# Kernel tuning notes

Measured on AMD Instinct MI355X. Metric: run time of the kernel, lower is better.

The kernel has to match this reference:

```python
import jax, jax.numpy as jnp
import numpy as np

EMBED_DIM = 1024
NUM_HEADS = 16


def setup_inputs() -> dict:
    key = jax.random.key(0)
    k_x, k_qw, k_qb, k_pw, k_bias, k_mask = jax.random.split(key, 6)
    B, N, C = 2, 2048, EMBED_DIM
    x = jax.random.normal(k_x, (B, N, C), dtype=jnp.float32)
    # torch Linear params: weight (out,in), bias (out,)
    qkv_w = jax.random.normal(k_qw, (3 * C, C), dtype=jnp.float32) * (C ** -0.5)
    qkv_b = jax.random.normal(k_qb, (3 * C,), dtype=jnp.float32) * 0.02
    proj_w = jax.random.normal(k_pw, (C, C), dtype=jnp.float32) * (C ** -0.5)
    proj_b = jnp.zeros((C,), dtype=jnp.float32)
    # nn.Parameter(torch.zeros(H,1,1)); small noise so the bias is non-trivial
    physics_bias = jax.random.normal(k_bias, (NUM_HEADS, 1, 1), dtype=jnp.float32) * 0.01
    physics_mask = jax.random.randint(k_mask, (B, 1, N, N), 0, 2).astype(jnp.int32)
    return {"x": x, "qkv_w": qkv_w, "qkv_b": qkv_b, "proj_w": proj_w,
            "proj_b": proj_b, "physics_bias": physics_bias,
            "physics_mask": physics_mask}


def reference(x, qkv_w, qkv_b, proj_w, proj_b, physics_bias, physics_mask):
    B, N, C = x.shape
    H = NUM_HEADS
    Dh = C // H
    # fused QKV projection: (B,N,3C) -> (B,N,3,H,Dh)
    qkv = (x @ qkv_w.T + qkv_b).reshape(B, N, 3, H, Dh)
    q = jnp.transpose(qkv[:, :, 0], (0, 2, 1, 3))  # (B,H,N,Dh)
    k = jnp.transpose(qkv[:, :, 1], (0, 2, 1, 3))
    v = jnp.transpose(qkv[:, :, 2], (0, 2, 1, 3))
    scale = Dh ** -0.5
    attn = jnp.einsum('bhnd,bhmd->bhnm', q, k) * scale  # (B,H,N,N)
    attn = attn + physics_bias  # (H,1,1) broadcasts per head
    attn = jnp.where(physics_mask == 0, -jnp.inf, attn)
    attn = jax.nn.softmax(attn, axis=-1)
    out = jnp.einsum('bhnm,bhmd->bhnd', attn, v)  # (B,H,N,Dh)
    out = jnp.transpose(out, (0, 2, 1, 3)).reshape(B, N, C)
    return out @ proj_w.T + proj_b
```

## Files before the change

### kernel.cpp

```cpp
#include <hip/hip_runtime.h>
#include <hip/hip_bf16.h>
#include <stdint.h>
#include <math.h>


typedef __bf16 bf16;
typedef __bf16 bf16x8 __attribute__((ext_vector_type(8)));
typedef __bf16 bf16x4 __attribute__((ext_vector_type(4)));
typedef float f32x4 __attribute__((ext_vector_type(4)));
typedef float f32x16 __attribute__((ext_vector_type(16)));

#define MFMA(a,b,c) __builtin_amdgcn_mfma_f32_16x16x32_bf16((a),(b),(c),0,0,0)
#define MFMA32(a,b,c) __builtin_amdgcn_mfma_f32_32x32x16_bf16((a),(b),(c),0,0,0)
#define L2E 1.44269504f

#if __has_builtin(__builtin_amdgcn_exp2f)
#define EXP2(x) __builtin_amdgcn_exp2f(x)
#else
#define EXP2(x) exp2f(x)
#endif

__device__ __forceinline__ void async16(const void* g, void* l) {
  __builtin_amdgcn_global_load_lds(
      (const __attribute__((address_space(1))) void*)g,
      (__attribute__((address_space(3))) void*)l, 16, 0, 0);
}

template <bool F32>
__device__ __forceinline__ bf16x8 ld8(const void* base, size_t off) {
  if constexpr (F32) {
    const float* p = (const float*)base + off;
    float4 u = *(const float4*)p;
    float4 v = *(const float4*)(p + 4);
    bf16x8 r;
    r[0] = (bf16)u.x; r[1] = (bf16)u.y; r[2] = (bf16)u.z; r[3] = (bf16)u.w;
    r[4] = (bf16)v.x; r[5] = (bf16)v.y; r[6] = (bf16)v.z; r[7] = (bf16)v.w;
    return r;
  } else {
    return *(const bf16x8*)((const bf16*)base + off);
  }
}

__global__ __launch_bounds__(256) void prep(const int* __restrict__ mask,
                                            unsigned long long* __restrict__ mbg,
                                            const float* __restrict__ x, bf16* __restrict__ xb,
                                            const float* __restrict__ qw, bf16* __restrict__ qwb,
                                            const float* __restrict__ pw, bf16* __restrict__ pwb) {
  int bid = blockIdx.x, tid = threadIdx.x;
  if (bid < 4096) {
    int lane = tid & 63, wv = tid >> 6;
    const int* mrow = mask + (size_t)bid * 2048;
#pragma unroll
    for (int i = 0; i < 8; ++i) {
      int w = wv * 8 + i;
      unsigned long long bal = __ballot(mrow[w * 64 + lane] != 0);
      if (lane == 0) mbg[(size_t)bid * 32 + w] = bal;
    }
  } else if (bid < 6144) {
    size_t i = ((size_t)(bid - 4096) * 256 + tid) * 8;
    *(bf16x8*)&xb[i] = ld8<true>(x, i);
  } else if (bid < 7680) {
    size_t i = ((size_t)(bid - 6144) * 256 + tid) * 8;
    *(bf16x8*)&qwb[i] = ld8<true>(qw, i);
  } else {
    size_t i = ((size_t)(bid - 7680) * 256 + tid) * 8;
    *(bf16x8*)&pwb[i] = ld8<true>(pw, i);
  }
}

template <bool AF32, bool BF32>
__device__ __forceinline__ void gemm_core(const void* __restrict__ A,
                                          const void* __restrict__ B,
                                          int m0, int n0,
                                          f32x4 acc[4][4],
                                          bf16* Al, bf16* Bl) {
  const int K = 1024;
  int tid = threadIdx.x, lane = tid & 63, wv = tid >> 6;
  int wm = wv & 1, wn = wv >> 1, g = lane >> 4, li = lane & 15;
  int r8 = lane >> 3, c8 = lane & 7;

  for (int kt = 0; kt < K; kt += 64) {
    if constexpr (!AF32 && !BF32) {
      const bf16* Ab = (const bf16*)A;
      const bf16* Bb = (const bf16*)B;
      __syncthreads();
#pragma unroll
      for (int i2 = 0; i2 < 4; ++i2) {
        int rb = wv * 32 + i2 * 8;
        async16(&Ab[(size_t)(m0 + rb + r8) * K + kt + c8 * 8], &Al[rb * 64]);
        async16(&Bb[(size_t)(n0 + rb + r8) * K + kt + c8 * 8], &Bl[rb * 64]);
      }
      __syncthreads();
    } else {
      bf16x8 ta[4], tb[4];
#pragma unroll
      for (int i2 = 0; i2 < 4; ++i2) {
        int row = wv * 32 + i2 * 8 + r8;
        ta[i2] = ld8<AF32>(A, (size_t)(m0 + row) * K + kt + c8 * 8);
        tb[i2] = ld8<BF32>(B, (size_t)(n0 + row) * K + kt + c8 * 8);
      }
      __syncthreads();
#pragma unroll
      for (int i2 = 0; i2 < 4; ++i2) {
        int row = wv * 32 + i2 * 8 + r8;
        *(bf16x8*)&Al[row * 64 + c8 * 8] = ta[i2];
        *(bf16x8*)&Bl[row * 64 + c8 * 8] = tb[i2];
      }
      __syncthreads();
    }
#pragma unroll
    for (int ks = 0; ks < 64; ks += 32) {
      bf16x8 af[4], bg[4];
#pragma unroll
      for (int i = 0; i < 4; ++i)
        af[i] = *(const bf16x8*)&Al[(wm * 64 + i * 16 + li) * 64 + ks + g * 8];
#pragma unroll
      for (int j = 0; j < 4; ++j)
        bg[j] = *(const bf16x8*)&Bl[(wn * 64 + j * 16 + li) * 64 + ks + g * 8];
#pragma unroll
      for (int i = 0; i < 4; ++i)
#pragma unroll
        for (int j = 0; j < 4; ++j)
          acc[i][j] = MFMA(af[i], bg[j], acc[i][j]);
    }
  }
}

__device__ __forceinline__ void epi_qk(f32x4 acc[4][4], int m0, int n0,
                                       const float* __restrict__ bias,
                                       bf16* __restrict__ qg, bf16* __restrict__ kg) {
  int lane = threadIdx.x & 63, wv = threadIdx.x >> 6;
  int wm = wv & 1, wn = wv >> 1, g = lane >> 4, li = lane & 15;
#pragma unroll
  for (int i = 0; i < 4; ++i) {
    int o = m0 + wm * 64 + i * 16 + g * 4;
    int s = o >> 10, h = (o >> 6) & 15, d = o & 63;
    float sc = s ? 1.0f : 0.125f * L2E;
    float b0 = bias[o], b1 = bias[o + 1], b2 = bias[o + 2], b3 = bias[o + 3];
    bf16* dstb = s ? kg : qg;
#pragma unroll
    for (int j = 0; j < 4; ++j) {
      int t = n0 + wn * 64 + j * 16 + li;
      int b = t >> 11, n = t & 2047;
      ushort4 pk;
      ((bf16*)&pk)[0] = (bf16)((acc[i][j][0] + b0) * sc);
      ((bf16*)&pk)[1] = (bf16)((acc[i][j][1] + b1) * sc);
      ((bf16*)&pk)[2] = (bf16)((acc[i][j][2] + b2) * sc);
      ((bf16*)&pk)[3] = (bf16)((acc[i][j][3] + b3) * sc);
      *(ushort4*)&dstb[(((size_t)b * 16 + h) * 2048 + n) * 64 + d] = pk;
    }
  }
}

__device__ __forceinline__ void epi_v(f32x4 acc[4][4], int m0, int n0,
                                      const float* __restrict__ bias,
                                      bf16* __restrict__ vtg) {
  int lane = threadIdx.x & 63, wvv = threadIdx.x >> 6;
  int wm = wvv & 1, wn = wvv >> 1, g = lane >> 4, li = lane & 15;
#pragma unroll
  for (int i = 0; i < 4; ++i) {
    int t = m0 + wm * 64 + i * 16 + g * 4;
    int b = t >> 11, n = t & 2047;
#pragma unroll
    for (int j = 0; j < 4; ++j) {
      int ov = n0 + wn * 64 + j * 16 + li;
      int h = ov >> 6, d = ov & 63;
      float bv = bias[ov];
      ushort4 pk;
      ((bf16*)&pk)[0] = (bf16)(acc[i][j][0] + bv);
      ((bf16*)&pk)[1] = (bf16)(acc[i][j][1] + bv);
      ((bf16*)&pk)[2] = (bf16)(acc[i][j][2] + bv);
      ((bf16*)&pk)[3] = (bf16)(acc[i][j][3] + bv);
      *(ushort4*)&vtg[(((size_t)b * 16 + h) * 64 + d) * 2048 + n] = pk;
    }
  }
}

__global__ __launch_bounds__(256) void gemm_qkv(const bf16* __restrict__ xb,
                                                const bf16* __restrict__ qwb,
                                                const float* __restrict__ bias,
                                                bf16* __restrict__ qg,
                                                bf16* __restrict__ kg,
                                                bf16* __restrict__ vtg) {
  __shared__ bf16 Al[128 * 64], Bl[128 * 64];
  f32x4 acc[4][4];
#pragma unroll
  for (int i = 0; i < 4; ++i)
#pragma unroll
    for (int j = 0; j < 4; ++j) acc[i][j] = (f32x4){0.f, 0.f, 0.f, 0.f};
  int bid = blockIdx.x;
  if (bid < 512) {
    int m0 = (bid >> 5) * 128, n0 = (bid & 31) * 128;
    gemm_core<false, false>(qwb, xb, m0, n0, acc, Al, Bl);
    epi_qk(acc, m0, n0, bias, qg, kg);
  } else {
    int vb = bid - 512;
    int m0 = (vb >> 3) * 128, n0 = (vb & 7) * 128;
    gemm_core<false, false>(xb, qwb + (size_t)2048 * 1024, m0, n0, acc, Al, Bl);
    epi_v(acc, m0, n0, bias + 2048, vtg);
  }
}

__global__ __launch_bounds__(256) void gemm_qk_f(const float* __restrict__ x,
                                                 const float* __restrict__ w,
                                                 const float* __restrict__ bias,
                                                 bf16* __restrict__ qg,
                                                 bf16* __restrict__ kg) {
  __shared__ bf16 Al[128 * 64], Bl[128 * 64];
  f32x4 acc[4][4];
#pragma unroll
  for (int i = 0; i < 4; ++i)
#pragma unroll
    for (int j = 0; j < 4; ++j) acc[i][j] = (f32x4){0.f, 0.f, 0.f, 0.f};
  int m0 = blockIdx.y * 128, n0 = blockIdx.x * 128;
  gemm_core<true, true>(w, x, m0, n0, acc, Al, Bl);
  epi_qk(acc, m0, n0, bias, qg, kg);
}
__global__ __launch_bounds__(256) void gemm_v_f(const float* __restrict__ x,
                                                const float* __restrict__ wv_,
                                                const float* __restrict__ bias,
                                                bf16* __restrict__ vtg) {
  __shared__ bf16 Al[128 * 64], Bl[128 * 64];
  f32x4 acc[4][4];
#pragma unroll
  for (int i = 0; i < 4; ++i)
#pragma unroll
    for (int j = 0; j < 4; ++j) acc[i][j] = (f32x4){0.f, 0.f, 0.f, 0.f};
  int m0 = blockIdx.y * 128, n0 = blockIdx.x * 128;
  gemm_core<true, true>(x, wv_, m0, n0, acc, Al, Bl);
  epi_v(acc, m0, n0, bias, vtg);
}
__global__ __launch_bounds__(256) void mask_bits(const int* __restrict__ mask,
                                                 unsigned long long* __restrict__ mbg) {
  int row = blockIdx.x, lane = threadIdx.x & 63, wv = threadIdx.x >> 6;
  const int* mrow = mask + (size_t)row * 2048;
#pragma unroll
  for (int i = 0; i < 8; ++i) {
    int w = wv * 8 + i;
    unsigned long long bal = __ballot(mrow[w * 64 + lane] != 0);
    if (lane == 0) mbg[(size_t)row * 32 + w] = bal;
  }
}

__global__ __launch_bounds__(512, 4) void flash_attn(
    const bf16* __restrict__ qg, const bf16* __restrict__ kg,
    const bf16* __restrict__ vtg, const unsigned long long* __restrict__ mbg,
    bf16* __restrict__ G) {
  __shared__ __align__(16) char smem[51712];

  int tid = threadIdx.x, lane = tid & 63, wv8 = tid >> 6;
  int grp = wv8 >> 2, wg = wv8 & 3;
  int cl = lane & 31, hi = lane >> 5;
  int r8 = lane >> 3, c8 = lane & 7;
  int q0 = blockIdx.x * 128;
  int bh = blockIdx.y, b = bh >> 4;
  const bf16* qbase = qg + (size_t)bh * 2048 * 64;
  const bf16* kbase = kg + (size_t)bh * 2048 * 64;
  const bf16* vbase = vtg + (size_t)bh * 64 * 2048;
  bf16* Kl = (bf16*)(smem + grp * 16384);
  bf16* Vl = (bf16*)(smem + grp * 16384 + 8192);

  int qrow = q0 + wg * 32 + cl;
  bf16x8 qf[4];
#pragma unroll
  for (int kd = 0; kd < 4; ++kd)
    qf[kd] = *(const bf16x8*)&qbase[(size_t)qrow * 64 + kd * 16 + hi * 8];
  const unsigned long long* mrow = mbg + (size_t)(b * 2048 + qrow) * 32;

  f32x16 accO0, accO1;
#pragma unroll
  for (int e = 0; e < 16; ++e) { accO0[e] = 0.f; accO1[e] = 0.f; }
  float lsum = 0.f;

  int srow0 = wg * 16 + r8, srow1 = wg * 16 + 8 + r8;
  int sw0 = (srow0 & 7) << 4, sw1 = (srow1 & 7) << 4;
  int ve0 = ((c8 >> 1) * 16 + (c8 & 1) * 4) * 2;
  int ve1 = ve0 + 16;
  int swr = (cl & 7) << 4;

  int nf = grp * 64;
  bf16x8 tk0 = *(const bf16x8*)&kbase[(size_t)(nf + srow0) * 64 + c8 * 8];
  bf16x8 tk1 = *(const bf16x8*)&kbase[(size_t)(nf + srow1) * 64 + c8 * 8];
  bf16x8 tv0 = *(const bf16x8*)&vbase[(size_t)srow0 * 2048 + nf + c8 * 8];
  bf16x8 tv1 = *(const bf16x8*)&vbase[(size_t)srow1 * 2048 + nf + c8 * 8];
  unsigned long long mw = mrow[grp];

  for (int t = 0; t < 16; ++t) {
    int it = 2 * t + grp;
    unsigned long long mwc = mw;
    __syncthreads();
    {
      *(bf16x8*)((char*)Kl + srow0 * 128 + ((c8 * 16) ^ sw0)) = tk0;
      *(bf16x8*)((char*)Kl + srow1 * 128 + ((c8 * 16) ^ sw1)) = tk1;
      bf16x4 lo, hh;
#pragma unroll
      for (int r = 0; r < 4; ++r) { lo[r] = tv0[r]; hh[r] = tv0[r + 4]; }
      *(bf16x4*)((char*)Vl + srow0 * 128 + (ve0 ^ sw0)) = lo;
      *(bf16x4*)((char*)Vl + srow0 * 128 + (ve1 ^ sw0)) = hh;
#pragma unroll
      for (int r = 0; r < 4; ++r) { lo[r] = tv1[r]; hh[r] = tv1[r + 4]; }
      *(bf16x4*)((char*)Vl + srow1 * 128 + (ve0 ^ sw1)) = lo;
      *(bf16x4*)((char*)Vl + srow1 * 128 + (ve1 ^ sw1)) = hh;
    }
    __syncthreads();

    int n1 = ((it + 2) & 31) * 64;
    tk0 = *(const bf16x8*)&kbase[(size_t)(n1 + srow0) * 64 + c8 * 8];
    tk1 = *(const bf16x8*)&kbase[(size_t)(n1 + srow1) * 64 + c8 * 8];
    tv0 = *(const bf16x8*)&vbase[(size_t)srow0 * 2048 + n1 + c8 * 8];
    tv1 = *(const bf16x8*)&vbase[(size_t)srow1 * 2048 + n1 + c8 * 8];
    mw = mrow[(it + 2) & 31];

    f32x16 accS0, accS1;
#pragma unroll
    for (int e = 0; e < 16; ++e) { accS0[e] = 0.f; accS1[e] = 0.f; }
#pragma unroll
    for (int kd = 0; kd < 4; ++kd) {
      int cb = (kd * 32 + hi * 16) ^ swr;
      bf16x8 kf0 = *(const bf16x8*)((char*)Kl + cl * 128 + cb);
      bf16x8 kf1 = *(const bf16x8*)((char*)Kl + (32 + cl) * 128 + cb);
      accS0 = MFMA32(kf0, qf[kd], accS0);
      accS1 = MFMA32(kf1, qf[kd], accS1);
    }

    unsigned dw[16];
#pragma unroll
    for (int nb = 0; nb < 2; ++nb) {
      unsigned mql = (unsigned)(mwc >> (nb * 32));
#pragma unroll
      for (int j = 0; j < 4; ++j) {
        float s0 = nb ? accS1[4 * j + 0] : accS0[4 * j + 0];
        float s1 = nb ? accS1[4 * j + 1] : accS0[4 * j + 1];
        float s2 = nb ? accS1[4 * j + 2] : accS0[4 * j + 2];
        float s3 = nb ? accS1[4 * j + 3] : accS0[4 * j + 3];
        unsigned m4 = (mql >> (j * 8 + hi * 4)) & 0xFu;
        float p0 = (m4 & 1u) ? EXP2(s0) : 0.f;
        float p1 = (m4 & 2u) ? EXP2(s1) : 0.f;
        float p2 = (m4 & 4u) ? EXP2(s2) : 0.f;
        float p3 = (m4 & 8u) ? EXP2(s3) : 0.f;
        lsum += (p0 + p1) + (p2 + p3);
        unsigned lo2, hi2;
        ((bf16*)&lo2)[0] = (bf16)p0; ((bf16*)&lo2)[1] = (bf16)p1;
        ((bf16*)&hi2)[0] = (bf16)p2; ((bf16*)&hi2)[1] = (bf16)p3;
        dw[nb * 8 + 2 * j] = lo2;
        dw[nb * 8 + 2 * j + 1] = hi2;
      }
    }

#pragma unroll
    for (int kk = 0; kk < 4; ++kk) {
      union { unsigned u[4]; bf16x8 v; } pa;
#pragma unroll
      for (int t2 = 0; t2 < 4; ++t2) pa.u[t2] = dw[kk * 4 + t2];
      int cb = (kk * 32 + hi * 16) ^ swr;
      bf16x8 vf0 = *(const bf16x8*)((char*)Vl + cl * 128 + cb);
      bf16x8 vf1 = *(const bf16x8*)((char*)Vl + (32 + cl) * 128 + cb);
      accO0 = MFMA32(vf0, pa.v, accO0);
      accO1 = MFMA32(vf1, pa.v, accO1);
    }
  }

  float ltot = lsum + __shfl_xor(lsum, 32);

  __syncthreads();
  float* oc = (float*)(smem + wg * 8192);
  float* lbuf = (float*)(smem + 32768);
  int osw = (cl & 7) << 4;
  if (grp == 1) {
#pragma unroll
    for (int j = 0; j < 4; ++j) {
      f32x4 qa, qb;
#pragma unroll
      for (int r = 0; r < 4; ++r) { qa[r] = accO0[4 * j + r]; qb[r] = accO1[4 * j + r]; }
      int dby = j * 32 + hi * 16;
      *(f32x4*)((char*)oc + cl * 256 + (dby ^ osw)) = qa;
      *(f32x4*)((char*)oc + cl * 256 + ((dby + 128) ^ osw)) = qb;
    }
    if (hi == 0) lbuf[wg * 32 + cl] = ltot;
  }
  __syncthreads();
  if (grp == 1) return;

  float lt2 = ltot + lbuf[wg * 32 + cl];
  float inv = 1.0f / fmaxf(lt2, 1e-37f);
#pragma unroll
  for (int j = 0; j < 4; ++j) {
    int dby = j * 32 + hi * 16;
    f32x4 qa = *(const f32x4*)((char*)oc + cl * 256 + (dby ^ osw));
    f32x4 qb = *(const f32x4*)((char*)oc + cl * 256 + ((dby + 128) ^ osw));
#pragma unroll
    for (int r = 0; r < 4; ++r) {
      accO0[4 * j + r] = (accO0[4 * j + r] + qa[r]) * inv;
      accO1[4 * j + r] = (accO1[4 * j + r] + qb[r]) * inv;
    }
  }

  bf16* ow = (bf16*)(smem + 33280) + wg * (32 * 72);
#pragma unroll
  for (int db = 0; db < 2; ++db) {
#pragma unroll
    for (int jq = 0; jq < 4; ++jq) {
      ushort4 pk;
      ((bf16*)&pk)[0] = (bf16)(db ? accO1[4 * jq + 0] : accO0[4 * jq + 0]);
      ((bf16*)&pk)[1] = (bf16)(db ? accO1[4 * jq + 1] : accO0[4 * jq + 1]);
      ((bf16*)&pk)[2] = (bf16)(db ? accO1[4 * jq + 2] : accO0[4 * jq + 2]);
      ((bf16*)&pk)[3] = (bf16)(db ? accO1[4 * jq + 3] : accO0[4 * jq + 3]);
      int dbase = db * 32 + jq * 8 + hi * 4;
      *(ushort4*)&ow[cl * 72 + dbase] = pk;
    }
  }

  int ql = lane >> 1, part = lane & 1;
  size_t tok = (size_t)b * 2048 + q0 + wg * 32 + ql;
  bf16* dst = G + tok * 1024 + (bh & 15) * 64 + part * 32;
  const bf16* src = &ow[ql * 72 + part * 32];
#pragma unroll
  for (int j = 0; j < 4; ++j)
    *(bf16x8*)&dst[j * 8] = *(const bf16x8*)&src[j * 8];
}

__global__ __launch_bounds__(256) void gemm_proj_n(const bf16* __restrict__ G,
                                                   const bf16* __restrict__ w,
                                                   const float* __restrict__ bias,
                                                   float* __restrict__ out) {
  __shared__ bf16 Al[128 * 64], Bl[64 * 64];
  const int K = 1024;
  int tid = threadIdx.x, lane = tid & 63, wv = tid >> 6;
  int wm = wv & 1, wn = wv >> 1, g = lane >> 4, li = lane & 15;
  int r8 = lane >> 3, c8 = lane & 7;
  int m0 = blockIdx.y * 128, n0 = blockIdx.x * 64;

  f32x4 acc[4][2];
#pragma unroll
  for (int i = 0; i < 4; ++i)
#pragma unroll
    for (int j = 0; j < 2; ++j) acc[i][j] = (f32x4){0.f, 0.f, 0.f, 0.f};

  for (int kt = 0; kt < K; kt += 64) {
    __syncthreads();
#pragma unroll
    for (int i2 = 0; i2 < 4; ++i2) {
      int rb = wv * 32 + i2 * 8;
      async16(&w[(size_t)(m0 + rb + r8) * K + kt + c8 * 8], &Al[rb * 64]);
    }
#pragma unroll
    for (int i2 = 0; i2 < 2; ++i2) {
      int rb = wv * 16 + i2 * 8;
      async16(&G[(size_t)(n0 + rb + r8) * K + kt + c8 * 8], &Bl[rb * 64]);
    }
    __syncthreads();
#pragma unroll
    for (int ks = 0; ks < 64; ks += 32) {
      bf16x8 af[4], bg[2];
#pragma unroll
      for (int i = 0; i < 4; ++i)
        af[i] = *(const bf16x8*)&Al[(wm * 64 + i * 16 + li) * 64 + ks + g * 8];
#pragma unroll
      for (int j = 0; j < 2; ++j)
        bg[j] = *(const bf16x8*)&Bl[(wn * 32 + j * 16 + li) * 64 + ks + g * 8];
#pragma unroll
      for (int i = 0; i < 4; ++i)
#pragma unroll
        for (int j = 0; j < 2; ++j)
          acc[i][j] = MFMA(af[i], bg[j], acc[i][j]);
    }
  }

#pragma unroll
  for (int i = 0; i < 4; ++i) {
    int ch = m0 + wm * 64 + i * 16 + g * 4;
    float b0 = bias[ch], b1 = bias[ch + 1], b2 = bias[ch + 2], b3 = bias[ch + 3];
#pragma unroll
    for (int j = 0; j < 2; ++j) {
      int t = n0 + wn * 32 + j * 16 + li;
      float4 pk = make_float4(acc[i][j][0] + b0, acc[i][j][1] + b1,
                              acc[i][j][2] + b2, acc[i][j][3] + b3);
      *(float4*)&out[(size_t)t * 1024 + ch] = pk;
    }
  }
}

__global__ __launch_bounds__(256) void gemm_proj_f(const bf16* __restrict__ G,
                                                   const float* __restrict__ w,
                                                   const float* __restrict__ bias,
                                                   float* __restrict__ out) {
  __shared__ bf16 Al[128 * 64], Bl[128 * 64];
  f32x4 acc[4][4];
#pragma unroll
  for (int i = 0; i < 4; ++i)
#pragma unroll
    for (int j = 0; j < 4; ++j) acc[i][j] = (f32x4){0.f, 0.f, 0.f, 0.f};
  int m0 = blockIdx.y * 128, n0 = blockIdx.x * 128;
  gemm_core<true, false>(w, G, m0, n0, acc, Al, Bl);

  int lane = threadIdx.x & 63, wv = threadIdx.x >> 6;
  int wm = wv & 1, wn = wv >> 1, g = lane >> 4, li = lane & 15;
#pragma unroll
  for (int i = 0; i < 4; ++i) {
    int ch = m0 + wm * 64 + i * 16 + g * 4;
    float b0 = bias[ch], b1 = bias[ch + 1], b2 = bias[ch + 2], b3 = bias[ch + 3];
#pragma unroll
    for (int j = 0; j < 4; ++j) {
      int t = n0 + wn * 64 + j * 16 + li;
      float4 pk = make_float4(acc[i][j][0] + b0, acc[i][j][1] + b1,
                              acc[i][j][2] + b2, acc[i][j][3] + b3);
      *(float4*)&out[(size_t)t * 1024 + ch] = pk;
    }
  }
}

extern "C" void kernel_launch(void* const* d_in, const int* in_sizes, int n_in,
                              void* d_out, int out_size, void* d_ws, size_t ws_size,
                              hipStream_t stream) {
  const float* x      = (const float*)d_in[0];
  const float* qkv_w  = (const float*)d_in[1];
  const float* qkv_b  = (const float*)d_in[2];
  const float* proj_w = (const float*)d_in[3];
  const float* proj_b = (const float*)d_in[4];
  const int* mask     = (const int*)d_in[6];
  float* out = (float*)d_out;

  const size_t MB = (size_t)1 << 20;
  char* ws = (char*)d_ws;
  bf16* qg  = (bf16*)(ws);
  bf16* kg  = (bf16*)(ws + 8 * MB);
  bf16* vtg = (bf16*)(ws + 16 * MB);
  bf16* xb  = (bf16*)(ws + 24 * MB);
  bf16* G   = (bf16*)(ws + 24 * MB);
  unsigned long long* mbg = (unsigned long long*)(ws + 32 * MB);
  bf16* qwb = (bf16*)(ws + 33 * MB);
  bf16* pwb = (bf16*)(ws + 39 * MB);
  bool pre = ws_size >= 41 * MB;

  if (pre) {
    prep<<<dim3(8192), dim3(256), 0, stream>>>(mask, mbg, x, xb, qkv_w, qwb,
                                               proj_w, pwb);
    gemm_qkv<<<dim3(768), dim3(256), 0, stream>>>(xb, qwb, qkv_b, qg, kg, vtg);
  } else {
    mask_bits<<<dim3(4096), dim3(256), 0, stream>>>(mask, mbg);
    gemm_qk_f<<<dim3(32, 16), dim3(256), 0, stream>>>(x, qkv_w, qkv_b, qg, kg);
    gemm_v_f<<<dim3(8, 32), dim3(256), 0, stream>>>(
        x, qkv_w + (size_t)2048 * 1024, qkv_b + 2048, vtg);
  }

  flash_attn<<<dim3(16, 32), dim3(512), 0, stream>>>(qg, kg, vtg, mbg, G);

  if (pre)
    gemm_proj_n<<<dim3(64, 8), dim3(256), 0, stream>>>(G, pwb, proj_b, out);
  else
    gemm_proj_f<<<dim3(32, 8), dim3(256), 0, stream>>>(G, proj_w, proj_b, out);
}
```

Before: 234.4 us.

## Async double-buffered K/V loads, branchless masking, and move mask/proj prep into QKV GEMM

Flash attention now stages K and V tiles into double-buffered LDS with direct global-to-LDS async loads, which removes the register round-trip and one barrier per iteration. It also computes masked probabilities branchlessly with a bitfield-extract mask, packs them with a single bf16 pair-convert instruction, and uses a permlane32 swap to build MFMA operands. The mask bit-packing and proj-weight conversion move out of the prep kernel and run as extra blocks of the QKV GEMM launch so they overlap with it. The attention grid is flattened and remapped so that neighbouring blocks share a query tile across heads. LDS use grows from about 51 KB to 66 KB, which may reduce occupancy.

```diff
diff --git a/kernel.cpp b/kernel.cpp
--- a/kernel.cpp
+++ b/kernel.cpp
@@ -20,10 +20,40 @@
 #define EXP2(x) exp2f(x)
 #endif
 
+#if __has_builtin(__builtin_amdgcn_sbfe)
+#define SBFE1(x,o) __builtin_amdgcn_sbfe((int)(x), (int)(o), 1)
+#else
+#define SBFE1(x,o) (((int)(((unsigned)(x)) << (31 - (o)))) >> 31)
+#endif
+
 __device__ __forceinline__ void async16(const void* g, void* l) {
   __builtin_amdgcn_global_load_lds(
       (const __attribute__((address_space(1))) void*)g,
       (__attribute__((address_space(3))) void*)l, 16, 0, 0);
+}
+
+__device__ __forceinline__ unsigned cvt_pk_bf16(float a, float b) {
+  unsigned r;
+  asm("v_cvt_pk_bf16_f32 %0, %1, %2" : "=v"(r) : "v"(a), "v"(b));
+  return r;
+}
+
+__device__ __forceinline__ float maskf(float p, unsigned m, int pos) {
+  int sm = SBFE1(m, pos);
+  return __uint_as_float(__float_as_uint(p) & (unsigned)sm);
+}
+
+__device__ __forceinline__ void lane32_swap(unsigned a, unsigned b,
+                                            unsigned& x, unsigned& y, int hi) {
+#if __has_builtin(__builtin_amdgcn_permlane32_swap)
+  auto r = __builtin_amdgcn_permlane32_swap((int)a, (int)b, false, false);
+  x = (unsigned)r[0];
+  y = (unsigned)r[1];
+#else
+  unsigned pa_ = __shfl_xor(a, 32), pb_ = __shfl_xor(b, 32);
+  x = hi ? pb_ : a;
+  y = hi ? b : pa_;
+#endif
 }
 
 template <bool F32>
@@ -41,30 +71,15 @@
   }
 }
 
-__global__ __launch_bounds__(256) void prep(const int* __restrict__ mask,
-                                            unsigned long long* __restrict__ mbg,
-                                            const float* __restrict__ x, bf16* __restrict__ xb,
-                                            const float* __restrict__ qw, bf16* __restrict__ qwb,
-                                            const float* __restrict__ pw, bf16* __restrict__ pwb) {
+__global__ __launch_bounds__(256) void prep(const float* __restrict__ x, bf16* __restrict__ xb,
+                                            const float* __restrict__ qw, bf16* __restrict__ qwb) {
   int bid = blockIdx.x, tid = threadIdx.x;
-  if (bid < 4096) {
-    int lane = tid & 63, wv = tid >> 6;
-    const int* mrow = mask + (size_t)bid * 2048;
-#pragma unroll
-    for (int i = 0; i < 8; ++i) {
-      int w = wv * 8 + i;
-      unsigned long long bal = __ballot(mrow[w * 64 + lane] != 0);
-      if (lane == 0) mbg[(size_t)bid * 32 + w] = bal;
-    }
-  } else if (bid < 6144) {
-    size_t i = ((size_t)(bid - 4096) * 256 + tid) * 8;
+  if (bid < 2048) {
+    size_t i = ((size_t)bid * 256 + tid) * 8;
     *(bf16x8*)&xb[i] = ld8<true>(x, i);
-  } else if (bid < 7680) {
-    size_t i = ((size_t)(bid - 6144) * 256 + tid) * 8;
+  } else {
+    size_t i = ((size_t)(bid - 2048) * 256 + tid) * 8;
     *(bf16x8*)&qwb[i] = ld8<true>(qw, i);
-  } else {
-    size_t i = ((size_t)(bid - 7680) * 256 + tid) * 8;
-    *(bf16x8*)&pwb[i] = ld8<true>(pw, i);
   }
 }
 
@@ -181,14 +196,34 @@
                                                 const float* __restrict__ bias,
                                                 bf16* __restrict__ qg,
                                                 bf16* __restrict__ kg,
-                                                bf16* __restrict__ vtg) {
+                                                bf16* __restrict__ vtg,
+                                                const int* __restrict__ mask,
+                                                unsigned long long* __restrict__ mbg,
+                                                const float* __restrict__ pw,
+                                                bf16* __restrict__ pwb) {
   __shared__ bf16 Al[128 * 64], Bl[128 * 64];
+  int bid = blockIdx.x, tid = threadIdx.x;
+  if (bid >= 768) {
+    if (bid < 4864) {
+      int row = bid - 768, lane = tid & 63, wvv = tid >> 6;
+      const int* mrow = mask + (size_t)row * 2048;
+#pragma unroll
+      for (int i = 0; i < 8; ++i) {
+        int w = wvv * 8 + i;
+        unsigned long long bal = __ballot(mrow[w * 64 + lane] != 0);
+        if (lane == 0) mbg[(size_t)row * 32 + w] = bal;
+      }
+    } else {
+      size_t i = ((size_t)(bid - 4864) * 256 + tid) * 8;
+      *(bf16x8*)&pwb[i] = ld8<true>(pw, i);
+    }
+    return;
+  }
   f32x4 acc[4][4];
 #pragma unroll
   for (int i = 0; i < 4; ++i)
 #pragma unroll
     for (int j = 0; j < 4; ++j) acc[i][j] = (f32x4){0.f, 0.f, 0.f, 0.f};
-  int bid = blockIdx.x;
   if (bid < 512) {
     int m0 = (bid >> 5) * 128, n0 = (bid & 31) * 128;
     gemm_core<false, false>(qwb, xb, m0, n0, acc, Al, Bl);
@@ -246,70 +281,69 @@
     const bf16* __restrict__ qg, const bf16* __restrict__ kg,
     const bf16* __restrict__ vtg, const unsigned long long* __restrict__ mbg,
     bf16* __restrict__ G) {
-  __shared__ __align__(16) char smem[51712];
+  __shared__ __align__(16) char smem[66048];
 
   int tid = threadIdx.x, lane = tid & 63, wv8 = tid >> 6;
   int grp = wv8 >> 2, wg = wv8 & 3;
   int cl = lane & 31, hi = lane >> 5;
-  int r8 = lane >> 3, c8 = lane & 7;
-  int q0 = blockIdx.x * 128;
-  int bh = blockIdx.y, b = bh >> 4;
+  int sblk = blockIdx.x;
+  int rest = sblk >> 3;
+  int bh = ((rest >> 4) << 3) | (sblk & 7);
+  int q0 = (rest & 15) * 128;
+  int b = bh >> 4;
+
   const bf16* qbase = qg + (size_t)bh * 2048 * 64;
-  const bf16* kbase = kg + (size_t)bh * 2048 * 64;
-  const bf16* vbase = vtg + (size_t)bh * 64 * 2048;
-  bf16* Kl = (bf16*)(smem + grp * 16384);
-  bf16* Vl = (bf16*)(smem + grp * 16384 + 8192);
+  const char* kgc = (const char*)(kg + (size_t)bh * 2048 * 64);
+  const char* vgc = (const char*)(vtg + (size_t)bh * 64 * 2048);
 
   int qrow = q0 + wg * 32 + cl;
   bf16x8 qf[4];
 #pragma unroll
   for (int kd = 0; kd < 4; ++kd)
     qf[kd] = *(const bf16x8*)&qbase[(size_t)qrow * 64 + kd * 16 + hi * 8];
-  const unsigned long long* mrow = mbg + (size_t)(b * 2048 + qrow) * 32;
+
+  int ln8 = lane >> 3;
+  int kcol = ((lane & 7) << 4) ^ ((ln8 & 7) << 4);
+  int koff = (grp * 64 + wg * 16 + ln8) * 128 + kcol;
+  int voff = (wg * 16 + ln8) * 4096 + grp * 128 + kcol;
+  const char* mB = (const char*)mbg;
+  unsigned moff = (unsigned)(((b * 2048 + qrow) * 32 + grp) * 8);
+  int ldsw = wg * 2048;
+
+  {
+    char* kl = smem + grp * 32768;
+    char* vl = kl + 8192;
+    async16(kgc + koff, kl + ldsw);
+    async16(kgc + koff + 1024, kl + ldsw + 1024);
+    async16(vgc + voff, vl + ldsw);
+    async16(vgc + voff + 32768, vl + ldsw + 1024);
+  }
+  unsigned long long mw_next = *(const unsigned long long*)(mB + moff);
 
   f32x16 accO0, accO1;
 #pragma unroll
   for (int e = 0; e < 16; ++e) { accO0[e] = 0.f; accO1[e] = 0.f; }
   float lsum = 0.f;
-
-  int srow0 = wg * 16 + r8, srow1 = wg * 16 + 8 + r8;
-  int sw0 = (srow0 & 7) << 4, sw1 = (srow1 & 7) << 4;
-  int ve0 = ((c8 >> 1) * 16 + (c8 & 1) * 4) * 2;
-  int ve1 = ve0 + 16;
   int swr = (cl & 7) << 4;
 
-  int nf = grp * 64;
-  bf16x8 tk0 = *(const bf16x8*)&kbase[(size_t)(nf + srow0) * 64 + c8 * 8];
-  bf16x8 tk1 = *(const bf16x8*)&kbase[(size_t)(nf + srow1) * 64 + c8 * 8];
-  bf16x8 tv0 = *(const bf16x8*)&vbase[(size_t)srow0 * 2048 + nf + c8 * 8];
-  bf16x8 tv1 = *(const bf16x8*)&vbase[(size_t)srow1 * 2048 + nf + c8 * 8];
-  unsigned long long mw = mrow[grp];
-
   for (int t = 0; t < 16; ++t) {
-    int it = 2 * t + grp;
-    unsigned long long mwc = mw;
-    __syncthreads();
-    {
-      *(bf16x8*)((char*)Kl + srow0 * 128 + ((c8 * 16) ^ sw0)) = tk0;
-      *(bf16x8*)((char*)Kl + srow1 * 128 + ((c8 * 16) ^ sw1)) = tk1;
-      bf16x4 lo, hh;
-#pragma unroll
-      for (int r = 0; r < 4; ++r) { lo[r] = tv0[r]; hh[r] = tv0[r + 4]; }
-      *(bf16x4*)((char*)Vl + srow0 * 128 + (ve0 ^ sw0)) = lo;
-      *(bf16x4*)((char*)Vl + srow0 * 128 + (ve1 ^ sw0)) = hh;
-#pragma unroll
-      for (int r = 0; r < 4; ++r) { lo[r] = tv1[r]; hh[r] = tv1[r + 4]; }
-      *(bf16x4*)((char*)Vl + srow1 * 128 + (ve0 ^ sw1)) = lo;
-      *(bf16x4*)((char*)Vl + srow1 * 128 + (ve1 ^ sw1)) = hh;
-    }
-    __syncthreads();
-
-    int n1 = ((it + 2) & 31) * 64;
-    tk0 = *(const bf16x8*)&kbase[(size_t)(n1 + srow0) * 64 + c8 * 8];
-    tk1 = *(const bf16x8*)&kbase[(size_t)(n1 + srow1) * 64 + c8 * 8];
-    tv0 = *(const bf16x8*)&vbase[(size_t)srow0 * 2048 + n1 + c8 * 8];
-    tv1 = *(const bf16x8*)&vbase[(size_t)srow1 * 2048 + n1 + c8 * 8];
-    mw = mrow[(it + 2) & 31];
+    asm volatile("s_waitcnt vmcnt(0)" ::: "memory");
+    __builtin_amdgcn_s_barrier();
+    __builtin_amdgcn_sched_barrier(0);
+    unsigned long long mwc = mw_next;
+    if (t < 15) {
+      koff += 16384; voff += 256; moff += 16;
+      char* kl = smem + grp * 32768 + (((t + 1) & 1) << 14);
+      char* vl = kl + 8192;
+      async16(kgc + koff, kl + ldsw);
+      async16(kgc + koff + 1024, kl + ldsw + 1024);
+      async16(vgc + voff, vl + ldsw);
+      async16(vgc + voff + 32768, vl + ldsw + 1024);
+      mw_next = *(const unsigned long long*)(mB + moff);
+    }
+    __builtin_amdgcn_sched_barrier(0);
+    const char* Kl = smem + grp * 32768 + ((t & 1) << 14);
+    const char* Vl = Kl + 8192;
 
     f32x16 accS0, accS1;
 #pragma unroll
@@ -317,8 +351,8 @@
 #pragma unroll
     for (int kd = 0; kd < 4; ++kd) {
       int cb = (kd * 32 + hi * 16) ^ swr;
-      bf16x8 kf0 = *(const bf16x8*)((char*)Kl + cl * 128 + cb);
-      bf16x8 kf1 = *(const bf16x8*)((char*)Kl + (32 + cl) * 128 + cb);
+      bf16x8 kf0 = *(const bf16x8*)(Kl + cl * 128 + cb);
+      bf16x8 kf1 = *(const bf16x8*)(Kl + (32 + cl) * 128 + cb);
       accS0 = MFMA32(kf0, qf[kd], accS0);
       accS1 = MFMA32(kf1, qf[kd], accS1);
     }
@@ -329,32 +363,27 @@
       unsigned mql = (unsigned)(mwc >> (nb * 32));
 #pragma unroll
       for (int j = 0; j < 4; ++j) {
-        float s0 = nb ? accS1[4 * j + 0] : accS0[4 * j + 0];
-        float s1 = nb ? accS1[4 * j + 1] : accS0[4 * j + 1];
-        float s2 = nb ? accS1[4 * j + 2] : accS0[4 * j + 2];
-        float s3 = nb ? accS1[4 * j + 3] : accS0[4 * j + 3];
-        unsigned m4 = (mql >> (j * 8 + hi * 4)) & 0xFu;
-        float p0 = (m4 & 1u) ? EXP2(s0) : 0.f;
-        float p1 = (m4 & 2u) ? EXP2(s1) : 0.f;
-        float p2 = (m4 & 4u) ? EXP2(s2) : 0.f;
-        float p3 = (m4 & 8u) ? EXP2(s3) : 0.f;
+        int pos = j * 8 + hi * 4;
+        float p0 = EXP2(nb ? accS1[4 * j + 0] : accS0[4 * j + 0]);
+        float p1 = EXP2(nb ? accS1[4 * j + 1] : accS0[4 * j + 1]);
+        float p2 = EXP2(nb ? accS1[4 * j + 2] : accS0[4 * j + 2]);
+        float p3 = EXP2(nb ? accS1[4 * j + 3] : accS0[4 * j + 3]);
+        p0 = maskf(p0, mql, pos);     p1 = maskf(p1, mql, pos + 1);
+        p2 = maskf(p2, mql, pos + 2); p3 = maskf(p3, mql, pos + 3);
         lsum += (p0 + p1) + (p2 + p3);
-        unsigned lo2, hi2;
-        ((bf16*)&lo2)[0] = (bf16)p0; ((bf16*)&lo2)[1] = (bf16)p1;
-        ((bf16*)&hi2)[0] = (bf16)p2; ((bf16*)&hi2)[1] = (bf16)p3;
-        dw[nb * 8 + 2 * j] = lo2;
-        dw[nb * 8 + 2 * j + 1] = hi2;
+        dw[nb * 8 + 2 * j]     = cvt_pk_bf16(p0, p1);
+        dw[nb * 8 + 2 * j + 1] = cvt_pk_bf16(p2, p3);
       }
     }
 
 #pragma unroll
     for (int kk = 0; kk < 4; ++kk) {
       union { unsigned u[4]; bf16x8 v; } pa;
-#pragma unroll
-      for (int t2 = 0; t2 < 4; ++t2) pa.u[t2] = dw[kk * 4 + t2];
+      lane32_swap(dw[4 * kk], dw[4 * kk + 2], pa.u[0], pa.u[2], hi);
+      lane32_swap(dw[4 * kk + 1], dw[4 * kk + 3], pa.u[1], pa.u[3], hi);
       int cb = (kk * 32 + hi * 16) ^ swr;
-      bf16x8 vf0 = *(const bf16x8*)((char*)Vl + cl * 128 + cb);
-      bf16x8 vf1 = *(const bf16x8*)((char*)Vl + (32 + cl) * 128 + cb);
+      bf16x8 vf0 = *(const bf16x8*)(Vl + cl * 128 + cb);
+      bf16x8 vf1 = *(const bf16x8*)(Vl + (32 + cl) * 128 + cb);
       accO0 = MFMA32(vf0, pa.v, accO0);
       accO1 = MFMA32(vf1, pa.v, accO1);
     }
@@ -364,7 +393,7 @@
 
   __syncthreads();
   float* oc = (float*)(smem + wg * 8192);
-  float* lbuf = (float*)(smem + 32768);
+  float* lbuf = (float*)(smem + 65536);
   int osw = (cl & 7) << 4;
   if (grp == 1) {
 #pragma unroll
@@ -395,7 +424,7 @@
     }
   }
 
-  bf16* ow = (bf16*)(smem + 33280) + wg * (32 * 72);
+  bf16* ow = (bf16*)(smem + wg * 8192);
 #pragma unroll
   for (int db = 0; db < 2; ++db) {
 #pragma unroll
@@ -533,9 +562,9 @@
   bool pre = ws_size >= 41 * MB;
 
   if (pre) {
-    prep<<<dim3(8192), dim3(256), 0, stream>>>(mask, mbg, x, xb, qkv_w, qwb,
-                                               proj_w, pwb);
-    gemm_qkv<<<dim3(768), dim3(256), 0, stream>>>(xb, qwb, qkv_b, qg, kg, vtg);
+    prep<<<dim3(3584), dim3(256), 0, stream>>>(x, xb, qkv_w, qwb);
+    gemm_qkv<<<dim3(5376), dim3(256), 0, stream>>>(xb, qwb, qkv_b, qg, kg, vtg,
+                                                   mask, mbg, proj_w, pwb);
   } else {
     mask_bits<<<dim3(4096), dim3(256), 0, stream>>>(mask, mbg);
     gemm_qk_f<<<dim3(32, 16), dim3(256), 0, stream>>>(x, qkv_w, qkv_b, qg, kg);
@@ -543,7 +572,7 @@
         x, qkv_w + (size_t)2048 * 1024, qkv_b + 2048, vtg);
   }
 
-  flash_attn<<<dim3(16, 32), dim3(512), 0, stream>>>(qg, kg, vtg, mbg, G);
+  flash_attn<<<dim3(512), dim3(512), 0, stream>>>(qg, kg, vtg, mbg, G);
 
   if (pre)
     gemm_proj_n<<<dim3(64, 8), dim3(256), 0, stream>>>(G, pwb, proj_b, out);
```

New measurement: 246.3 us. 1.05x slower.
